# Optimization experiments

Measured on AMD Instinct MI355X. Metric: run time of the kernel, lower is better.

Reference implementation:

```python
import jax, jax.numpy as jnp
import numpy as np

B, N, H = 16, 1024, 1024


def setup_inputs() -> dict:
    key = jax.random.key(0)
    ks = jax.random.split(key, 12)
    inv = 1.0 / np.sqrt(H)
    inp = {
        "x": jax.random.normal(ks[0], (B, N, H), jnp.float32),
        "atom_graph": jax.random.normal(ks[1], (B, N, N), jnp.float32),
        "variable_graph": jax.random.normal(ks[2], (B, N, N), jnp.float32),
        "Wq": jax.random.uniform(ks[3], (H, H), jnp.float32, -inv, inv),
        "bq": jax.random.uniform(ks[4], (H,), jnp.float32, -inv, inv),
        "Wk": jax.random.uniform(ks[5], (H, H), jnp.float32, -inv, inv),
        "bk": jax.random.uniform(ks[6], (H,), jnp.float32, -inv, inv),
        "Wv": jax.random.uniform(ks[7], (H, H), jnp.float32, -inv, inv),
        "bv": jax.random.uniform(ks[8], (H,), jnp.float32, -inv, inv),
        "predicate_pos": jax.random.randint(ks[9], (B, N), 0, 2, jnp.int32),
        "variable_tags": jax.random.randint(ks[10], (B, N), 0, 4, jnp.int32),
    }
    return inp


def _path_pool(h, predicate_pos):
    # h: [B,N,H]; predicate_pos: [B,N] in {0,1}
    b, n, d = h.shape
    i = jnp.arange(n)
    # pos[i-2] (value irrelevant for i<2, those branches handled explicitly)
    pp2 = jnp.pad(predicate_pos, ((0, 0), (2, 0)))[:, :n]  # [B,N]
    # window [s, e): i==0 -> [0,2); i==1 -> [0,3); pos[i-2]==1 -> [i,i+2); else [i-1,i+2)
    s = jnp.where(i < 2, 0, jnp.where(pp2 == 1, i, i - 1))  # [B,N]
    e = jnp.where(i == 0, 2, jnp.where(i == 1, 3, i + 2))    # [N]
    e = jnp.minimum(e, n)
    e = jnp.broadcast_to(e, (b, n))
    # prefix sums along node dim with a leading zero row -> windowed means via gather
    cs = jnp.concatenate([jnp.zeros((b, 1, d), h.dtype), jnp.cumsum(h, axis=1)], axis=1)  # [B,N+1,H]
    win_sum = (jnp.take_along_axis(cs, e[:, :, None], axis=1)
               - jnp.take_along_axis(cs, s[:, :, None], axis=1))  # [B,N,H]
    means = win_sum / (e - s)[:, :, None].astype(h.dtype)
    mask = (predicate_pos == 1).astype(h.dtype)  # [B,N]
    item = (means * mask[:, :, None]).sum(axis=1) / mask.sum(axis=1)[:, None]  # [B,H]
    return jnp.broadcast_to(item[:, None, :], (b, n, d))


def reference(x, atom_graph, variable_graph, Wq, bq, Wk, bk, Wv, bv,
              predicate_pos, variable_tags):
    scale = x.shape[-1] ** (-0.5)
    q = (x @ Wq.T + bq) * scale
    k = x @ Wk.T + bk
    v = x @ Wv.T + bv
    att = jnp.einsum("bnh,bmh->bnm", q, k) + atom_graph + variable_graph
    att = jax.nn.softmax(att, axis=-1)  # dropout is identity in eval
    h = jnp.einsum("bnm,bmh->bnh", att, v)
    return _path_pool(h, predicate_pos)
```

## Files before the change

### kernel.cpp

```cpp
#include <hip/hip_runtime.h>
#include <hip/hip_bf16.h>

#define BATCH 16
#define SEQ   1024
#define DIM   1024

typedef __attribute__((ext_vector_type(8))) short bf16x8;
typedef __attribute__((ext_vector_type(4))) float f32x4;
typedef __attribute__((ext_vector_type(4))) unsigned short us4;

__device__ __forceinline__ float bfu2f(unsigned short u) {
  union { unsigned int i; float f; } c; c.i = ((unsigned int)u) << 16; return c.f;
}
__device__ __forceinline__ unsigned short f2bfu(float f) {
  union { float f; unsigned int i; } c; c.f = f;
  return (unsigned short)((c.i + 0x7FFFu + ((c.i >> 16) & 1u)) >> 16);
}
__device__ __forceinline__ void async16(void* lds, const void* g) {
  __builtin_amdgcn_global_load_lds(
      (const __attribute__((address_space(1))) unsigned int*)g,
      (__attribute__((address_space(3))) unsigned int*)lds, 16, 0, 0);
}

__global__ void cast_xw_kernel(const float* __restrict__ x, const float* __restrict__ Wv,
                               unsigned short* __restrict__ xb,
                               unsigned short* __restrict__ Wvb, int x4) {
  int i = blockIdx.x * blockDim.x + threadIdx.x;
  const float* in; unsigned short* out; int j;
  if (i < x4) { in = x; out = xb; j = i; }
  else { in = Wv; out = Wvb; j = i - x4; }
  f32x4 v = ((const f32x4*)in)[j];
  us4 o;
  o[0] = f2bfu(v[0]); o[1] = f2bfu(v[1]); o[2] = f2bfu(v[2]); o[3] = f2bfu(v[3]);
  ((us4*)out)[j] = o;
}

__global__ void castT_kernel(const float* __restrict__ Wq, const float* __restrict__ Wk,
                             unsigned short* __restrict__ WqT,
                             unsigned short* __restrict__ WkT) {
  const float* in = (blockIdx.z == 0) ? Wq : Wk;
  unsigned short* out = (blockIdx.z == 0) ? WqT : WkT;
  __shared__ float t[64][65];
  const int h0 = blockIdx.x * 64, i0 = blockIdx.y * 64;
  const int tid = threadIdx.x;
  const int sub = tid >> 4, c4 = tid & 15;
#pragma unroll
  for (int p = 0; p < 4; ++p) {
    const int row = p * 16 + sub;
    f32x4 v = *(const f32x4*)(in + (size_t)(h0 + row) * DIM + i0 + c4 * 4);
    t[row][c4 * 4 + 0] = v[0]; t[row][c4 * 4 + 1] = v[1];
    t[row][c4 * 4 + 2] = v[2]; t[row][c4 * 4 + 3] = v[3];
  }
  __syncthreads();
#pragma unroll
  for (int p = 0; p < 4; ++p) {
    const int orow = p * 16 + sub;
    us4 o;
    o[0] = f2bfu(t[c4 * 4 + 0][orow]);
    o[1] = f2bfu(t[c4 * 4 + 1][orow]);
    o[2] = f2bfu(t[c4 * 4 + 2][orow]);
    o[3] = f2bfu(t[c4 * 4 + 3][orow]);
    *(us4*)(out + (size_t)(i0 + orow) * DIM + h0 + c4 * 4) = o;
  }
}

__global__ void t12_kernel(const unsigned short* __restrict__ WqT,
                           const unsigned short* __restrict__ WkT,
                           const float* __restrict__ bq, const float* __restrict__ bk,
                           float* __restrict__ t1, float* __restrict__ t2) {
  const int y = blockIdx.y;
  const unsigned short* Wt = y ? WkT : WqT;
  const float* vec = y ? bq : bk;
  float* tout = y ? t2 : t1;
  const int wave = threadIdx.x >> 6, lane = threadIdx.x & 63;
  const int i = blockIdx.x * 4 + wave;
  const us4* wr = (const us4*)(Wt + (size_t)i * DIM);
  float s = 0.f;
#pragma unroll
  for (int t = 0; t < 4; ++t) {
    us4 w4 = wr[lane + 64 * t];
    f32x4 b4 = *(const f32x4*)(vec + (lane + 64 * t) * 4);
    s += bfu2f(w4[0]) * b4[0] + bfu2f(w4[1]) * b4[1] +
         bfu2f(w4[2]) * b4[2] + bfu2f(w4[3]) * b4[3];
  }
#pragma unroll
  for (int o = 32; o; o >>= 1) s += __shfl_down(s, o);
  if (lane == 0) tout[i] = s;
}

__global__ void ac_kernel(const unsigned short* __restrict__ xb,
                          const float* __restrict__ t1, const float* __restrict__ t2,
                          const float* __restrict__ bq, const float* __restrict__ bk,
                          float* __restrict__ a, float* __restrict__ c) {
  const float scale = 0.03125f;
  const int tid = threadIdx.x;
  const int wave = tid >> 6, lane = tid & 63;
  float dp = 0.f;
  for (int i = tid; i < DIM; i += 256) dp += bq[i] * bk[i];
#pragma unroll
  for (int o = 32; o; o >>= 1) dp += __shfl_down(dp, o);
  __shared__ float dred[4];
  if ((tid & 63) == 0) dred[tid >> 6] = dp;
  __syncthreads();
  const float d = dred[0] + dred[1] + dred[2] + dred[3];
  float t1r[16], t2r[16];
#pragma unroll
  for (int t = 0; t < 4; ++t) {
    f32x4 v1 = *(const f32x4*)(t1 + (lane + 64 * t) * 4);
    f32x4 v2 = *(const f32x4*)(t2 + (lane + 64 * t) * 4);
#pragma unroll
    for (int j = 0; j < 4; ++j) { t1r[t * 4 + j] = v1[j]; t2r[t * 4 + j] = v2[j]; }
  }
  for (int rr = 0; rr < 16; ++rr) {
    const int row = blockIdx.x * 64 + wave * 16 + rr;
    const us4* xr = (const us4*)(xb + (size_t)row * DIM);
    float sa = 0.f, sc = 0.f;
#pragma unroll
    for (int t = 0; t < 4; ++t) {
      us4 v = xr[lane + 64 * t];
#pragma unroll
      for (int j = 0; j < 4; ++j) {
        const float f = bfu2f(v[j]);
        sa += f * t1r[t * 4 + j];
        sc += f * t2r[t * 4 + j];
      }
    }
#pragma unroll
    for (int o = 32; o; o >>= 1) { sa += __shfl_down(sa, o); sc += __shfl_down(sc, o); }
    if (lane == 0) {
      a[row] = scale * (sa + d);
      c[row] = scale * sc;
    }
  }
}

__global__ void pathw_kernel(const int* __restrict__ pos, float* __restrict__ w,
                             float* __restrict__ denom, float* __restrict__ zbias) {
  const int b = blockIdx.x;
  __shared__ int ps[SEQ];
  __shared__ int mcnt;
  const int tid = threadIdx.x;
  if (tid == 0) mcnt = 0;
  __syncthreads();
  if (b == 0)
    for (int i = tid; i < DIM; i += 256) zbias[i] = 0.f;
  for (int i = tid; i < SEQ; i += 256) {
    ps[i] = pos[b * SEQ + i];
    denom[b * SEQ + i] = 0.f;
  }
  __syncthreads();
  int c = 0;
  for (int i = tid; i < SEQ; i += 256) c += ps[i];
  for (int o = 32; o; o >>= 1) c += __shfl_down(c, o);
  if ((tid & 63) == 0) atomicAdd(&mcnt, c);
  __syncthreads();
  const float invM = 1.0f / (float)mcnt;
  for (int j = tid; j < SEQ; j += 256) {
    float a = 0.f;
#pragma unroll
    for (int di = -1; di <= 1; ++di) {
      int i = j + di;
      if (i < 0 || i >= SEQ) continue;
      if (!ps[i]) continue;
      int s, e;
      if (i < 2) { s = 0; e = (i == 0) ? 2 : 3; }
      else { s = (ps[i - 2] == 1) ? i : (i - 1); e = i + 2; if (e > SEQ) e = SEQ; }
      if (s <= j && j < e) a += 1.0f / (float)(e - s);
    }
    w[b * SEQ + j] = a * invM;
  }
}

__global__ void proj_gemm(const unsigned short* __restrict__ A,
                          const unsigned short* __restrict__ W,
                          const float* __restrict__ bias, float alpha,
                          unsigned short* __restrict__ C, int M, int N, int K)
{
  __shared__ __align__(16) char smem[16896];
  unsigned short* As = (unsigned short*)smem;
  unsigned short* Bs = (unsigned short*)(smem + 8192);
  float* Sl = (float*)smem;
  const int tid = threadIdx.x;
  const int wave = tid >> 6, lane = tid & 63;
  const int lr = lane & 15, lg = lane >> 4;
  const int wr = wave >> 1, wc = wave & 1;
  const int flat = blockIdx.x + gridDim.x * blockIdx.y;
  const int q8 = (gridDim.x * gridDim.y) >> 3;
  const int t = (flat & 7) * q8 + (flat >> 3);
  const int m0 = (t / gridDim.y) * 128;
  const int n0 = (t % gridDim.y) * 128;
  const int off0 = tid * 16, off1 = 4096 + tid * 16;
  const int r0 = off0 >> 6, ke0 = (off0 >> 1) & 31;
  const int r1 = off1 >> 6, ke1 = (off1 >> 1) & 31;
  f32x4 acc[4][4] = {};
  for (int kk = 0; kk < K; kk += 32) {
    async16((char*)As + off0, A + (size_t)(m0 + r0) * K + kk + ke0);
    async16((char*)As + off1, A + (size_t)(m0 + r1) * K + kk + ke1);
    async16((char*)Bs + off0, W + (size_t)(n0 + r0) * K + kk + ke0);
    async16((char*)Bs + off1, W + (size_t)(n0 + r1) * K + kk + ke1);
    __syncthreads();
    bf16x8 af[4], bfv[4];
#pragma unroll
    for (int i = 0; i < 4; ++i) {
      af[i]  = *(const bf16x8*)((const char*)As + ((wr * 64 + i * 16 + lr) << 6) + (lg << 4));
      bfv[i] = *(const bf16x8*)((const char*)Bs + ((wc * 64 + i * 16 + lr) << 6) + (lg << 4));
    }
#pragma unroll
    for (int i = 0; i < 4; ++i)
#pragma unroll
      for (int j = 0; j < 4; ++j)
        acc[i][j] = __builtin_amdgcn_mfma_f32_16x16x32_bf16(af[i], bfv[j], acc[i][j], 0, 0, 0);
    __syncthreads();
  }
#pragma unroll
  for (int p = 0; p < 4; ++p) {
    __syncthreads();
    if (wr == (p >> 1)) {
      const int ibase = (p & 1) * 2;
#pragma unroll
      for (int ii = 0; ii < 2; ++ii) {
        const int i = ibase + ii;
#pragma unroll
        for (int j = 0; j < 4; ++j)
#pragma unroll
          for (int r = 0; r < 4; ++r)
            Sl[(ii * 16 + lg * 4 + r) * 132 + wc * 64 + j * 16 + lr] = acc[i][j][r];
      }
    }
    __syncthreads();
#pragma unroll
    for (int it = 0; it < 4; ++it) {
      const int v = tid + it * 256;
      const int lrow = v >> 5, c4 = v & 31;
      const int grow = m0 + p * 32 + lrow;
      const int col = n0 + c4 * 4;
      const f32x4 s4 = *(const f32x4*)(&Sl[lrow * 132 + c4 * 4]);
      const f32x4 b4 = *(const f32x4*)(bias + col);
      us4 o;
      o[0] = f2bfu((s4[0] + b4[0]) * alpha);
      o[1] = f2bfu((s4[1] + b4[1]) * alpha);
      o[2] = f2bfu((s4[2] + b4[2]) * alpha);
      o[3] = f2bfu((s4[3] + b4[3]) * alpha);
      *(us4*)(C + (size_t)grow * N + col) = o;
    }
  }
}

__global__ void qk_exp_kernel(const unsigned short* __restrict__ z,
                              const unsigned short* __restrict__ xb,
                              const float* __restrict__ ag,
                              const float* __restrict__ vg,
                              const float* __restrict__ av,
                              const float* __restrict__ cv,
                              unsigned short* __restrict__ E,
                              float* __restrict__ denom)
{
  __shared__ __align__(16) char smem[16896];
  unsigned short* As = (unsigned short*)smem;
  unsigned short* Bs = (unsigned short*)(smem + 8192);
  float* Sl = (float*)smem;
  const int flat = blockIdx.x + 8 * blockIdx.y + 64 * blockIdx.z;
  const int t = (flat & 7) * 128 + (flat >> 3);
  const int b = t >> 6;
  const int m0 = (t & 7) * 128;
  const int n0 = ((t >> 3) & 7) * 128;
  const unsigned short* Aq = z + ((size_t)b << 20);
  const unsigned short* Bk = xb + ((size_t)b << 20);
  const int tid = threadIdx.x;
  const int wave = tid >> 6, lane = tid & 63;
  const int lr = lane & 15, lg = lane >> 4;
  const int wr = wave >> 1, wc = wave & 1;
  const int off0 = tid * 16, off1 = 4096 + tid * 16;
  const int r0 = off0 >> 6, ke0 = (off0 >> 1) & 31;
  const int r1 = off1 >> 6, ke1 = (off1 >> 1) & 31;
  f32x4 acc[4][4] = {};
  for (int kk = 0; kk < DIM; kk += 32) {
    async16((char*)As + off0, Aq + (size_t)(m0 + r0) * DIM + kk + ke0);
    async16((char*)As + off1, Aq + (size_t)(m0 + r1) * DIM + kk + ke1);
    async16((char*)Bs + off0, Bk + (size_t)(n0 + r0) * DIM + kk + ke0);
    async16((char*)Bs + off1, Bk + (size_t)(n0 + r1) * DIM + kk + ke1);
    __syncthreads();
    bf16x8 af[4], bfv[4];
#pragma unroll
    for (int i = 0; i < 4; ++i) {
      af[i]  = *(const bf16x8*)((const char*)As + ((wr * 64 + i * 16 + lr) << 6) + (lg << 4));
      bfv[i] = *(const bf16x8*)((const char*)Bs + ((wc * 64 + i * 16 + lr) << 6) + (lg << 4));
    }
#pragma unroll
    for (int i = 0; i < 4; ++i)
#pragma unroll
      for (int j = 0; j < 4; ++j)
        acc[i][j] = __builtin_amdgcn_mfma_f32_16x16x32_bf16(af[i], bfv[j], acc[i][j], 0, 0, 0);
    __syncthreads();
  }
  const float* agb = ag + ((size_t)b << 20);
  const float* vgb = vg + ((size_t)b << 20);
  unsigned short* Eb = E + ((size_t)b << 20);
  float* dnb = denom + b * SEQ;
  const float* avb = av + b * SEQ;
  const float* cvb = cv + b * SEQ;
#pragma unroll
  for (int p = 0; p < 4; ++p) {
    __syncthreads();
    if (wr == (p >> 1)) {
      const int ibase = (p & 1) * 2;
#pragma unroll
      for (int ii = 0; ii < 2; ++ii) {
        const int i = ibase + ii;
#pragma unroll
        for (int j = 0; j < 4; ++j)
#pragma unroll
          for (int r = 0; r < 4; ++r)
            Sl[(ii * 16 + lg * 4 + r) * 132 + wc * 64 + j * 16 + lr] = acc[i][j][r];
      }
    }
    __syncthreads();
#pragma unroll
    for (int it = 0; it < 4; ++it) {
      const int v = tid + it * 256;
      const int lrow = v >> 5, c4 = v & 31;
      const int grow = m0 + p * 32 + lrow;
      const size_t base = (size_t)grow * SEQ + n0 + c4 * 4;
      const f32x4 a4 = *(const f32x4*)(agb + base);
      const f32x4 g4 = *(const f32x4*)(vgb + base);
      const f32x4 c4v = *(const f32x4*)(cvb + n0 + c4 * 4);
      const float arow = avb[grow];
      const f32x4 s4 = *(const f32x4*)(&Sl[lrow * 132 + c4 * 4]);
      const float e0 = __expf(s4[0] + a4[0] + g4[0] + arow + c4v[0]);
      const float e1 = __expf(s4[1] + a4[1] + g4[1] + arow + c4v[1]);
      const float e2 = __expf(s4[2] + a4[2] + g4[2] + arow + c4v[2]);
      const float e3 = __expf(s4[3] + a4[3] + g4[3] + arow + c4v[3]);
      us4 o;
      o[0] = f2bfu(e0); o[1] = f2bfu(e1); o[2] = f2bfu(e2); o[3] = f2bfu(e3);
      *(us4*)(Eb + base) = o;
      float rs = e0 + e1 + e2 + e3;
#pragma unroll
      for (int o2 = 16; o2; o2 >>= 1) rs += __shfl_down(rs, o2, 32);
      if ((tid & 31) == 0) atomicAdd(&dnb[grow], rs);
    }
  }
}

__global__ void wcolsum_part(const unsigned short* __restrict__ Mt,
                             const float* __restrict__ wv,
                             const float* __restrict__ dv,
                             const float* __restrict__ pin,
                             float* __restrict__ part) {
  const int b = blockIdx.z;
  const int nc = blockIdx.y;
  const int m = blockIdx.x * 256 + threadIdx.x;
  __shared__ float c[128];
  const int tid = threadIdx.x;
  if (tid < 128) {
    const int n = nc * 128 + tid;
    float cvw;
    if (pin) {
      cvw = 0.f;
#pragma unroll
      for (int j = 0; j < 8; ++j) cvw += pin[(size_t)((b * 8 + j) << 10) + n];
    } else {
      cvw = wv[b * SEQ + n];
      if (dv) cvw /= dv[b * SEQ + n];
    }
    c[tid] = cvw;
  }
  __syncthreads();
  const unsigned short* p = Mt + ((size_t)b << 20) + ((size_t)(nc * 128) << 10) + m;
  float acc = 0.f;
#pragma unroll 8
  for (int n = 0; n < 128; ++n) acc += c[n] * bfu2f(p[(size_t)n << 10]);
  part[(size_t)((b * 8 + nc) << 10) + m] = acc;
}

__global__ void wcolsum_reduce(const float* __restrict__ part, float* __restrict__ out) {
  const int b = blockIdx.y;
  const int m = blockIdx.x * 256 + threadIdx.x;
  float s = 0.f;
#pragma unroll
  for (int nc = 0; nc < 8; ++nc) s += part[(size_t)((b * 8 + nc) << 10) + m];
  out[b * SEQ + m] = s;
}

__global__ void item_kernel(const float* __restrict__ y, const float* __restrict__ part1,
                            const unsigned short* __restrict__ Wvb,
                            const float* __restrict__ bv, float* __restrict__ item) {
  const int b = blockIdx.x;
  const int hblk = blockIdx.y;
  __shared__ float ys[DIM];
  __shared__ float sred[4];
  const int tid = threadIdx.x;
  float part = 0.f;
  for (int i = tid; i < DIM; i += 256) ys[i] = y[b * DIM + i];
  for (int i = tid; i < 8 * SEQ; i += 256) part += part1[(size_t)(b * 8) * SEQ + i];
  for (int o = 32; o; o >>= 1) part += __shfl_down(part, o);
  if ((tid & 63) == 0) sred[tid >> 6] = part;
  __syncthreads();
  const float su = sred[0] + sred[1] + sred[2] + sred[3];
  const int wave = tid >> 6, lane = tid & 63;
  const int h = hblk * 4 + wave;
  const us4* wrow = (const us4*)(Wvb + (size_t)h * DIM);
  float acc = 0.f;
#pragma unroll
  for (int t = 0; t < 4; ++t) {
    us4 v = wrow[t * 64 + lane];
    const int d0 = (t * 64 + lane) * 4;
    acc += ys[d0] * bfu2f(v[0]) + ys[d0 + 1] * bfu2f(v[1]) +
           ys[d0 + 2] * bfu2f(v[2]) + ys[d0 + 3] * bfu2f(v[3]);
  }
  for (int o = 32; o; o >>= 1) acc += __shfl_down(acc, o);
  if (lane == 0) item[b * DIM + h] = acc + su * bv[h];
}

__global__ void bcast_kernel(const float* __restrict__ item, float* __restrict__ out) {
  const int b = blockIdx.y;
  const int n = blockIdx.x;
  const f32x4* src = (const f32x4*)(item + b * DIM);
  f32x4* dst = (f32x4*)(out + (((size_t)b * SEQ + n) << 10));
  dst[threadIdx.x] = src[threadIdx.x];
}

extern "C" void kernel_launch(void* const* d_in, const int* in_sizes, int n_in,
                              void* d_out, int out_size, void* d_ws, size_t ws_size,
                              hipStream_t stream) {
  const float* x    = (const float*)d_in[0];
  const float* ag   = (const float*)d_in[1];
  const float* vgr  = (const float*)d_in[2];
  const float* Wq   = (const float*)d_in[3];
  const float* bq   = (const float*)d_in[4];
  const float* Wk   = (const float*)d_in[5];
  const float* bk   = (const float*)d_in[6];
  const float* Wv   = (const float*)d_in[7];
  const float* bv   = (const float*)d_in[8];
  const int*   pos  = (const int*)d_in[9];
  float* out = (float*)d_out;

  char* ws = (char*)d_ws;
  size_t off = 0;
  auto alloc = [&](size_t bytes) { void* p = ws + off; off += (bytes + 255) & ~(size_t)255; return p; };
  const size_t BNH = (size_t)BATCH * SEQ * DIM;
  unsigned short* xb   = (unsigned short*)alloc(BNH * 2);
  unsigned short* zb   = (unsigned short*)alloc(BNH * 2);
  unsigned short* E    = (unsigned short*)alloc(BNH * 2);
  unsigned short* WqT  = (unsigned short*)alloc((size_t)DIM * DIM * 2);
  unsigned short* WkT  = (unsigned short*)alloc((size_t)DIM * DIM * 2);
  unsigned short* Wvb  = (unsigned short*)alloc((size_t)DIM * DIM * 2);
  unsigned short* Hb   = (unsigned short*)alloc((size_t)DIM * DIM * 2);
  float* w     = (float*)alloc((size_t)BATCH * SEQ * 4);
  float* denom = (float*)alloc((size_t)BATCH * SEQ * 4);
  float* av    = (float*)alloc((size_t)BATCH * SEQ * 4);
  float* cvv   = (float*)alloc((size_t)BATCH * SEQ * 4);
  float* t1    = (float*)alloc((size_t)DIM * 4);
  float* t2    = (float*)alloc((size_t)DIM * 4);
  float* zbias = (float*)alloc((size_t)DIM * 4);
  float* y     = (float*)alloc((size_t)BATCH * DIM * 4);
  float* item  = (float*)alloc((size_t)BATCH * DIM * 4);
  float* part1 = (float*)alloc((size_t)BATCH * 8 * SEQ * 4);
  float* part2 = (float*)alloc((size_t)BATCH * 8 * SEQ * 4);

  const float scale = 0.03125f;
  const int x4 = (int)(BNH / 4);

  cast_xw_kernel<<<(x4 + DIM * DIM / 4) / 256, 256, 0, stream>>>(x, Wv, xb, Wvb, x4);
  castT_kernel<<<dim3(16, 16, 2), 256, 0, stream>>>(Wq, Wk, WqT, WkT);

  pathw_kernel<<<BATCH, 256, 0, stream>>>(pos, w, denom, zbias);

  t12_kernel<<<dim3(256, 2), 256, 0, stream>>>(WqT, WkT, bq, bk, t1, t2);
  ac_kernel<<<256, 256, 0, stream>>>(xb, t1, t2, bq, bk, av, cvv);

  proj_gemm<<<dim3(8, 8), 256, 0, stream>>>(WkT, WqT, zbias, scale, Hb, DIM, DIM, DIM);

  proj_gemm<<<dim3(128, 8), 256, 0, stream>>>(xb, Hb, zbias, 1.0f, zb,
                                              BATCH * SEQ, DIM, DIM);

  qk_exp_kernel<<<dim3(8, 8, BATCH), 256, 0, stream>>>(zb, xb, ag, vgr, av, cvv, E, denom);

  wcolsum_part<<<dim3(4, 8, BATCH), 256, 0, stream>>>(E, w, denom, nullptr, part1);

  wcolsum_part<<<dim3(4, 8, BATCH), 256, 0, stream>>>(xb, nullptr, nullptr, part1, part2);
  wcolsum_reduce<<<dim3(4, BATCH), 256, 0, stream>>>(part2, y);

  item_kernel<<<dim3(BATCH, 256), 256, 0, stream>>>(y, part1, Wvb, bv, item);

  bcast_kernel<<<dim3(SEQ, BATCH), 256, 0, stream>>>(item, out);
}
```

Before: 232.1 us.

## Stage full score tile as bf16 in LDS and restructure weighted column-sum reductions

The QK epilogue now writes the whole 128x128 accumulator tile to LDS once as bf16 instead of four fp32 passes with barriers. It then batches the loads of atom_graph and variable_graph four-wide, so more global reads are in flight before the exp and store work. The weighted column-sum kernels are rewritten to use vectorized us4 loads over 64-row chunks, with a separate reduce kernel that also produces the per-batch scalar sum, so item_kernel no longer re-reduces the partials. Trade-offs are larger LDS use, which lowers occupancy, fewer blocks in the column-sum kernels, one extra launch, and bf16 rounding of the scores before exp.

```diff
diff --git a/kernel.cpp b/kernel.cpp
--- a/kernel.cpp
+++ b/kernel.cpp
@@ -255,10 +255,10 @@
                               unsigned short* __restrict__ E,
                               float* __restrict__ denom)
 {
-  __shared__ __align__(16) char smem[16896];
+  __shared__ __align__(16) char smem[33792];
   unsigned short* As = (unsigned short*)smem;
   unsigned short* Bs = (unsigned short*)(smem + 8192);
-  float* Sl = (float*)smem;
+  unsigned short* Slb = (unsigned short*)smem;
   const int flat = blockIdx.x + 8 * blockIdx.y + 64 * blockIdx.z;
   const int t = (flat & 7) * 128 + (flat >> 3);
   const int b = t >> 6;
@@ -293,6 +293,15 @@
         acc[i][j] = __builtin_amdgcn_mfma_f32_16x16x32_bf16(af[i], bfv[j], acc[i][j], 0, 0, 0);
     __syncthreads();
   }
+#pragma unroll
+  for (int i = 0; i < 4; ++i)
+#pragma unroll
+    for (int j = 0; j < 4; ++j)
+#pragma unroll
+      for (int r = 0; r < 4; ++r)
+        Slb[(wr * 64 + i * 16 + lg * 4 + r) * 132 + wc * 64 + j * 16 + lr] =
+            f2bfu(acc[i][j][r]);
+  __syncthreads();
   const float* agb = ag + ((size_t)b << 20);
   const float* vgb = vg + ((size_t)b << 20);
   unsigned short* Eb = E + ((size_t)b << 20);
@@ -300,102 +309,100 @@
   const float* avb = av + b * SEQ;
   const float* cvb = cv + b * SEQ;
 #pragma unroll
-  for (int p = 0; p < 4; ++p) {
-    __syncthreads();
-    if (wr == (p >> 1)) {
-      const int ibase = (p & 1) * 2;
-#pragma unroll
-      for (int ii = 0; ii < 2; ++ii) {
-        const int i = ibase + ii;
-#pragma unroll
-        for (int j = 0; j < 4; ++j)
-#pragma unroll
-          for (int r = 0; r < 4; ++r)
-            Sl[(ii * 16 + lg * 4 + r) * 132 + wc * 64 + j * 16 + lr] = acc[i][j][r];
-      }
-    }
-    __syncthreads();
-#pragma unroll
-    for (int it = 0; it < 4; ++it) {
-      const int v = tid + it * 256;
-      const int lrow = v >> 5, c4 = v & 31;
-      const int grow = m0 + p * 32 + lrow;
-      const size_t base = (size_t)grow * SEQ + n0 + c4 * 4;
-      const f32x4 a4 = *(const f32x4*)(agb + base);
-      const f32x4 g4 = *(const f32x4*)(vgb + base);
+  for (int bt = 0; bt < 4; ++bt) {
+    f32x4 a4[4], g4[4];
+    int lrow[4];
+    size_t basev[4];
+#pragma unroll
+    for (int q = 0; q < 4; ++q) {
+      const int v = tid + (bt * 4 + q) * 256;
+      lrow[q] = v >> 5;
+      const int c4 = v & 31;
+      basev[q] = (size_t)(m0 + lrow[q]) * SEQ + n0 + c4 * 4;
+      a4[q] = *(const f32x4*)(agb + basev[q]);
+      g4[q] = *(const f32x4*)(vgb + basev[q]);
+    }
+#pragma unroll
+    for (int q = 0; q < 4; ++q) {
+      const int v = tid + (bt * 4 + q) * 256;
+      const int c4 = v & 31;
       const f32x4 c4v = *(const f32x4*)(cvb + n0 + c4 * 4);
-      const float arow = avb[grow];
-      const f32x4 s4 = *(const f32x4*)(&Sl[lrow * 132 + c4 * 4]);
-      const float e0 = __expf(s4[0] + a4[0] + g4[0] + arow + c4v[0]);
-      const float e1 = __expf(s4[1] + a4[1] + g4[1] + arow + c4v[1]);
-      const float e2 = __expf(s4[2] + a4[2] + g4[2] + arow + c4v[2]);
-      const float e3 = __expf(s4[3] + a4[3] + g4[3] + arow + c4v[3]);
+      const float arow = avb[m0 + lrow[q]];
+      const us4 sv = *(const us4*)(&Slb[lrow[q] * 132 + c4 * 4]);
+      const float e0 = __expf(bfu2f(sv[0]) + a4[q][0] + g4[q][0] + arow + c4v[0]);
+      const float e1 = __expf(bfu2f(sv[1]) + a4[q][1] + g4[q][1] + arow + c4v[1]);
+      const float e2 = __expf(bfu2f(sv[2]) + a4[q][2] + g4[q][2] + arow + c4v[2]);
+      const float e3 = __expf(bfu2f(sv[3]) + a4[q][3] + g4[q][3] + arow + c4v[3]);
       us4 o;
       o[0] = f2bfu(e0); o[1] = f2bfu(e1); o[2] = f2bfu(e2); o[3] = f2bfu(e3);
-      *(us4*)(Eb + base) = o;
+      *(us4*)(Eb + basev[q]) = o;
       float rs = e0 + e1 + e2 + e3;
 #pragma unroll
       for (int o2 = 16; o2; o2 >>= 1) rs += __shfl_down(rs, o2, 32);
-      if ((tid & 31) == 0) atomicAdd(&dnb[grow], rs);
-    }
-  }
-}
-
-__global__ void wcolsum_part(const unsigned short* __restrict__ Mt,
-                             const float* __restrict__ wv,
-                             const float* __restrict__ dv,
-                             const float* __restrict__ pin,
-                             float* __restrict__ part) {
-  const int b = blockIdx.z;
-  const int nc = blockIdx.y;
-  const int m = blockIdx.x * 256 + threadIdx.x;
-  __shared__ float c[128];
-  const int tid = threadIdx.x;
-  if (tid < 128) {
-    const int n = nc * 128 + tid;
-    float cvw;
-    if (pin) {
-      cvw = 0.f;
-#pragma unroll
-      for (int j = 0; j < 8; ++j) cvw += pin[(size_t)((b * 8 + j) << 10) + n];
-    } else {
-      cvw = wv[b * SEQ + n];
-      if (dv) cvw /= dv[b * SEQ + n];
-    }
+      if ((tid & 31) == 0) atomicAdd(&dnb[m0 + lrow[q]], rs);
+    }
+  }
+}
+
+__global__ void wcol_kernel(const unsigned short* __restrict__ Mt,
+                            const float* __restrict__ wv,
+                            const float* __restrict__ dv,
+                            float* __restrict__ part) {
+  const int nc = blockIdx.x;
+  const int b = blockIdx.y;
+  const int tid = threadIdx.x;
+  __shared__ float c[64];
+  if (tid < 64) {
+    const int n = nc * 64 + tid;
+    float cvw = wv[b * SEQ + n];
+    if (dv) cvw /= dv[b * SEQ + n];
     c[tid] = cvw;
   }
   __syncthreads();
-  const unsigned short* p = Mt + ((size_t)b << 20) + ((size_t)(nc * 128) << 10) + m;
-  float acc = 0.f;
+  const unsigned short* p = Mt + ((size_t)b << 20) + ((size_t)(nc * 64) << 10) + tid * 4;
+  f32x4 acc = {0.f, 0.f, 0.f, 0.f};
 #pragma unroll 8
-  for (int n = 0; n < 128; ++n) acc += c[n] * bfu2f(p[(size_t)n << 10]);
-  part[(size_t)((b * 8 + nc) << 10) + m] = acc;
-}
-
-__global__ void wcolsum_reduce(const float* __restrict__ part, float* __restrict__ out) {
-  const int b = blockIdx.y;
-  const int m = blockIdx.x * 256 + threadIdx.x;
-  float s = 0.f;
-#pragma unroll
-  for (int nc = 0; nc < 8; ++nc) s += part[(size_t)((b * 8 + nc) << 10) + m];
-  out[b * SEQ + m] = s;
-}
-
-__global__ void item_kernel(const float* __restrict__ y, const float* __restrict__ part1,
+  for (int n = 0; n < 64; ++n) {
+    const us4 v = *(const us4*)(p + ((size_t)n << 10));
+    const float cn = c[n];
+    acc[0] += cn * bfu2f(v[0]); acc[1] += cn * bfu2f(v[1]);
+    acc[2] += cn * bfu2f(v[2]); acc[3] += cn * bfu2f(v[3]);
+  }
+  *(f32x4*)(part + (size_t)((b * 16 + nc) << 10) + tid * 4) = acc;
+}
+
+__global__ void wred_kernel(const float* __restrict__ part, float* __restrict__ vec,
+                            float* __restrict__ su) {
+  const int b = blockIdx.x;
+  const int tid = threadIdx.x;
+  f32x4 s = {0.f, 0.f, 0.f, 0.f};
+#pragma unroll
+  for (int nc = 0; nc < 16; ++nc) {
+    const f32x4 v = *(const f32x4*)(part + (size_t)((b * 16 + nc) << 10) + tid * 4);
+    s[0] += v[0]; s[1] += v[1]; s[2] += v[2]; s[3] += v[3];
+  }
+  *(f32x4*)(vec + b * SEQ + tid * 4) = s;
+  if (su) {
+    float ts = s[0] + s[1] + s[2] + s[3];
+#pragma unroll
+    for (int o = 32; o; o >>= 1) ts += __shfl_down(ts, o);
+    __shared__ float red[4];
+    if ((tid & 63) == 0) red[tid >> 6] = ts;
+    __syncthreads();
+    if (tid == 0) su[b] = red[0] + red[1] + red[2] + red[3];
+  }
+}
+
+__global__ void item_kernel(const float* __restrict__ y, const float* __restrict__ su,
                             const unsigned short* __restrict__ Wvb,
                             const float* __restrict__ bv, float* __restrict__ item) {
   const int b = blockIdx.x;
   const int hblk = blockIdx.y;
   __shared__ float ys[DIM];
-  __shared__ float sred[4];
-  const int tid = threadIdx.x;
-  float part = 0.f;
+  const int tid = threadIdx.x;
   for (int i = tid; i < DIM; i += 256) ys[i] = y[b * DIM + i];
-  for (int i = tid; i < 8 * SEQ; i += 256) part += part1[(size_t)(b * 8) * SEQ + i];
-  for (int o = 32; o; o >>= 1) part += __shfl_down(part, o);
-  if ((tid & 63) == 0) sred[tid >> 6] = part;
-  __syncthreads();
-  const float su = sred[0] + sred[1] + sred[2] + sred[3];
+  __syncthreads();
+  const float sub = su[b];
   const int wave = tid >> 6, lane = tid & 63;
   const int h = hblk * 4 + wave;
   const us4* wrow = (const us4*)(Wvb + (size_t)h * DIM);
@@ -408,7 +415,7 @@
            ys[d0 + 2] * bfu2f(v[2]) + ys[d0 + 3] * bfu2f(v[3]);
   }
   for (int o = 32; o; o >>= 1) acc += __shfl_down(acc, o);
-  if (lane == 0) item[b * DIM + h] = acc + su * bv[h];
+  if (lane == 0) item[b * DIM + h] = acc + sub * bv[h];
 }
 
 __global__ void bcast_kernel(const float* __restrict__ item, float* __restrict__ out) {
@@ -447,15 +454,16 @@
   unsigned short* Hb   = (unsigned short*)alloc((size_t)DIM * DIM * 2);
   float* w     = (float*)alloc((size_t)BATCH * SEQ * 4);
   float* denom = (float*)alloc((size_t)BATCH * SEQ * 4);
+  float* u     = (float*)alloc((size_t)BATCH * SEQ * 4);
   float* av    = (float*)alloc((size_t)BATCH * SEQ * 4);
   float* cvv   = (float*)alloc((size_t)BATCH * SEQ * 4);
   float* t1    = (float*)alloc((size_t)DIM * 4);
   float* t2    = (float*)alloc((size_t)DIM * 4);
   float* zbias = (float*)alloc((size_t)DIM * 4);
   float* y     = (float*)alloc((size_t)BATCH * DIM * 4);
+  float* su    = (float*)alloc((size_t)BATCH * 4);
   float* item  = (float*)alloc((size_t)BATCH * DIM * 4);
-  float* part1 = (float*)alloc((size_t)BATCH * 8 * SEQ * 4);
-  float* part2 = (float*)alloc((size_t)BATCH * 8 * SEQ * 4);
+  float* part  = (float*)alloc((size_t)BATCH * 16 * SEQ * 4);
 
   const float scale = 0.03125f;
   const int x4 = (int)(BNH / 4);
@@ -475,12 +483,13 @@
 
   qk_exp_kernel<<<dim3(8, 8, BATCH), 256, 0, stream>>>(zb, xb, ag, vgr, av, cvv, E, denom);
 
-  wcolsum_part<<<dim3(4, 8, BATCH), 256, 0, stream>>>(E, w, denom, nullptr, part1);
-
-  wcolsum_part<<<dim3(4, 8, BATCH), 256, 0, stream>>>(xb, nullptr, nullptr, part1, part2);
-  wcolsum_reduce<<<dim3(4, BATCH), 256, 0, stream>>>(part2, y);
-
-  item_kernel<<<dim3(BATCH, 256), 256, 0, stream>>>(y, part1, Wvb, bv, item);
+  wcol_kernel<<<dim3(16, BATCH), 256, 0, stream>>>(E, w, denom, part);
+  wred_kernel<<<BATCH, 256, 0, stream>>>(part, u, su);
+
+  wcol_kernel<<<dim3(16, BATCH), 256, 0, stream>>>(xb, u, nullptr, part);
+  wred_kernel<<<BATCH, 256, 0, stream>>>(part, y, nullptr);
+
+  item_kernel<<<dim3(BATCH, 256), 256, 0, stream>>>(y, su, Wvb, bv, item);
 
   bcast_kernel<<<dim3(SEQ, BATCH), 256, 0, stream>>>(item, out);
 }
```

Measured after the change: 222.8 us. 1.04x faster.
